# Optimization experiments

Hardware: AMD Instinct MI355X
Metric: run time of the kernel (lower is better)

Reference implementation:

```python
import jax, jax.numpy as jnp
import numpy as np

B, H, W, C = 8, 256, 256, 64
M1, M2 = 16, 16
WIDTH = 64
W_SCALE = 0.02  # mimics he-normal-ish init magnitude for complex spectral weights


def setup_inputs() -> dict:
    key = jax.random.key(0)
    k1, k2, k3 = jax.random.split(key, 3)
    x = jax.random.normal(k1, (B, H, W, C), dtype=jnp.float32)
    w_real = jax.random.normal(k2, (M1, M2, C, WIDTH), dtype=jnp.float32)
    w_imag = jax.random.normal(k3, (M1, M2, C, WIDTH), dtype=jnp.float32)
    return {"x": x, "w_real": w_real, "w_imag": w_imag}


def reference(x, w_real, w_imag):
    # complex spectral weights: (M1, M2, C_in, C_out)
    weights = (w_real + 1j * w_imag) * W_SCALE
    spatial = x.shape[1:-1]  # (H, W)
    # full real FFT over spatial axes -> (B, H, W//2+1, C) complex
    x_ft = jnp.fft.rfftn(x, axes=(1, 2))
    # truncate to low-frequency modes
    x_m = x_ft[:, :M1, :M2, :]  # (B, M1, M2, C)
    # per-mode channel mixing (broadcast-ellipsis einsum in the original)
    out_m = jnp.einsum("bxyi,xyio->bxyo", x_m, weights)  # (B, M1, M2, WIDTH)
    # zero-pad back to full spectral grid
    pad = ((0, 0), (0, x_ft.shape[1] - M1), (0, x_ft.shape[2] - M2), (0, 0))
    out_ft = jnp.pad(out_m, pad, mode="constant")
    # inverse real FFT back to spatial domain
    out = jnp.fft.irfftn(out_ft, s=spatial, axes=(1, 2))  # (B, H, W, WIDTH)
    return out
```

## Files before the change

### kernel.cpp

```cpp
#include <hip/hip_runtime.h>


#define NB 8
#define NH 256
#define NW 256
#define NC 64
#define NM 16
#define NO 64

__global__ __launch_bounds__(256) void k_dft_w(const float* __restrict__ x,
                                               float* __restrict__ Gr, float* __restrict__ Gi) {
  __shared__ float2 cs[256];
  const int t = threadIdx.x;
  {
    float s, c;
    sincospif((float)t * (1.0f / 128.0f), &s, &c);
    cs[t] = make_float2(c, s);
  }
  __syncthreads();
  const int b = blockIdx.x >> 7;
  const int h2 = blockIdx.x & 127;
  const int i4 = t & 15;
  const int hs = (t >> 4) & 1;
  const int kyq = t >> 5;
  const int ky0 = kyq * 2, ky1 = ky0 + 1;
  const int h = h2 * 2 + hs;
  const float* xp = x + ((size_t)(b * NH + h) * NW) * NC + i4 * 4;

  float4 ar0 = {0, 0, 0, 0}, ai0 = {0, 0, 0, 0}, ar1 = {0, 0, 0, 0}, ai1 = {0, 0, 0, 0};
  const float2 s0 = cs[ky0], s1 = cs[ky1];
  const float s0r = s0.x, s0i = -s0.y, s1r = s1.x, s1i = -s1.y;

  for (int wc = 0; wc < 8; ++wc) {
    const int w0 = wc * 32;
    const float2 v0 = cs[(ky0 * w0) & 255], v1 = cs[(ky1 * w0) & 255];
    float t0r = v0.x, t0i = -v0.y, t1r = v1.x, t1i = -v1.y;
#pragma unroll 8
    for (int w = 0; w < 32; ++w) {
      const float4 xv = *(const float4*)(xp + (size_t)(w0 + w) * NC);
      ar0.x += t0r * xv.x; ar0.y += t0r * xv.y; ar0.z += t0r * xv.z; ar0.w += t0r * xv.w;
      ai0.x += t0i * xv.x; ai0.y += t0i * xv.y; ai0.z += t0i * xv.z; ai0.w += t0i * xv.w;
      ar1.x += t1r * xv.x; ar1.y += t1r * xv.y; ar1.z += t1r * xv.z; ar1.w += t1r * xv.w;
      ai1.x += t1i * xv.x; ai1.y += t1i * xv.y; ai1.z += t1i * xv.z; ai1.w += t1i * xv.w;
      float n0r = t0r * s0r - t0i * s0i, n0i = t0r * s0i + t0i * s0r;
      float n1r = t1r * s1r - t1i * s1i, n1i = t1r * s1i + t1i * s1r;
      t0r = n0r; t0i = n0i; t1r = n1r; t1i = n1i;
    }
  }
  const size_t g0 = ((size_t)(b * NM + ky0) * NH + h) * NC + i4 * 4;
  const size_t g1 = ((size_t)(b * NM + ky1) * NH + h) * NC + i4 * 4;
  *(float4*)(Gr + g0) = ar0; *(float4*)(Gi + g0) = ai0;
  *(float4*)(Gr + g1) = ar1; *(float4*)(Gi + g1) = ai1;
}

__global__ __launch_bounds__(256) void k_dft_h(const float* __restrict__ Gr, const float* __restrict__ Gi,
                                               float* __restrict__ Xpr, float* __restrict__ Xpi) {
  __shared__ float2 cs[256];
  __shared__ float gr[32 * 64];
  __shared__ float gi[32 * 64];
  const int t = threadIdx.x;
  {
    float s, c;
    sincospif((float)t * (1.0f / 128.0f), &s, &c);
    cs[t] = make_float2(c, s);
  }
  const int b = blockIdx.x >> 7;
  const int ky = (blockIdx.x >> 3) & 15;
  const int hc = blockIdx.x & 7;
  const float* grs = Gr + ((size_t)(b * NM + ky) * NH + hc * 32) * NC;
  const float* gis = Gi + ((size_t)(b * NM + ky) * NH + hc * 32) * NC;
#pragma unroll
  for (int r = 0; r < 2; ++r) {
    ((float4*)gr)[r * 256 + t] = ((const float4*)grs)[r * 256 + t];
    ((float4*)gi)[r * 256 + t] = ((const float4*)gis)[r * 256 + t];
  }
  __syncthreads();
  const int i4 = t & 15;
  const int kx = t >> 4;
  float4 xr = {0, 0, 0, 0}, xi = {0, 0, 0, 0};
  const float2 sv = cs[kx];
  const float str = sv.x, sti = -sv.y;
  const float2 tv = cs[(kx * hc * 32) & 255];
  float twr = tv.x, twi = -tv.y;
#pragma unroll 4
  for (int hh = 0; hh < 32; ++hh) {
    const float4 g_r = *(const float4*)&gr[hh * 64 + i4 * 4];
    const float4 g_i = *(const float4*)&gi[hh * 64 + i4 * 4];
    xr.x += twr * g_r.x - twi * g_i.x;
    xr.y += twr * g_r.y - twi * g_i.y;
    xr.z += twr * g_r.z - twi * g_i.z;
    xr.w += twr * g_r.w - twi * g_i.w;
    xi.x += twr * g_i.x + twi * g_r.x;
    xi.y += twr * g_i.y + twi * g_r.y;
    xi.z += twr * g_i.z + twi * g_r.z;
    xi.w += twr * g_i.w + twi * g_r.w;
    const float nr = twr * str - twi * sti;
    const float ni = twr * sti + twi * str;
    twr = nr; twi = ni;
  }
  const size_t o = ((size_t)((hc * NM + kx) * NM + ky) * NB + b) * NC + i4 * 4;
  *(float4*)(Xpr + o) = xr;
  *(float4*)(Xpi + o) = xi;
}

__global__ __launch_bounds__(256) void k_mix(const float* __restrict__ Xpr, const float* __restrict__ Xpi,
                                             const float* __restrict__ w_real, const float* __restrict__ w_imag,
                                             float2* __restrict__ om) {
  __shared__ float wr_s[64 * 32];
  __shared__ float wi_s[64 * 32];
  __shared__ float2 xc[8 * 64];
  const int t = threadIdx.x;
  const int kx = blockIdx.x >> 5;
  const int ky = (blockIdx.x >> 1) & 15;
  const int oh = blockIdx.x & 1;
  const size_t wb = (size_t)(kx * NM + ky) * 4096 + oh * 32;
#pragma unroll
  for (int r = 0; r < 2; ++r) {
    const int idx = r * 256 + t;
    const int i = idx >> 3, f = idx & 7;
    *(float4*)&wr_s[i * 32 + f * 4] = *(const float4*)(w_real + wb + (size_t)i * 64 + f * 4);
    *(float4*)&wi_s[i * 32 + f * 4] = *(const float4*)(w_imag + wb + (size_t)i * 64 + f * 4);
  }
#pragma unroll
  for (int r = 0; r < 2; ++r) {
    const int idx = r * 256 + t;
    const size_t base = (size_t)(kx * NM + ky) * 512 + idx;
    float sr = 0.f, si = 0.f;
#pragma unroll
    for (int hc = 0; hc < 8; ++hc) {
      sr += Xpr[base + (size_t)hc * 131072];
      si += Xpi[base + (size_t)hc * 131072];
    }
    xc[idx] = make_float2(sr, si);
  }
  __syncthreads();
  const int o = t & 31;
  const int b = t >> 5;
  float r0 = 0.f, i0 = 0.f;
#pragma unroll 8
  for (int i = 0; i < 64; ++i) {
    const float2 xv = xc[b * 64 + i];
    const float wrv = wr_s[i * 32 + o];
    const float wiv = wi_s[i * 32 + o];
    r0 += xv.x * wrv - xv.y * wiv;
    i0 += xv.x * wiv + xv.y * wrv;
  }
  const float sc = (ky == 0 ? 1.0f : 2.0f) * (0.02f / 65536.0f);
  om[((size_t)(b * NM + kx) * NM + ky) * NO + oh * 32 + o] = make_float2(r0 * sc, i0 * sc);
}

__global__ __launch_bounds__(256) void k_idft_w(const float2* __restrict__ om, float2* __restrict__ Zc) {
  __shared__ float2 cs[256];
  const int t = threadIdx.x;
  {
    float s, c;
    sincospif((float)t * (1.0f / 128.0f), &s, &c);
    cs[t] = make_float2(c, s);
  }
  __syncthreads();
  const int b = blockIdx.x >> 7;
  const int kx = (blockIdx.x >> 3) & 15;
  const int wq = blockIdx.x & 7;
  const int o = t & 63;
  const int wg = t >> 6;
  float mr[16], mi[16];
  const size_t base = ((size_t)(b * NM + kx) * NM) * NO + o;
#pragma unroll
  for (int ky = 0; ky < NM; ++ky) {
    const float2 v = om[base + ky * NO];
    mr[ky] = v.x; mi[ky] = v.y;
  }
#pragma unroll
  for (int j = 0; j < 8; ++j) {
    const int w = wq * 32 + wg * 8 + j;
    const float2 st = cs[w];
    float twr = 1.0f, twi = 0.0f;
    float zr = 0.0f, zi = 0.0f;
#pragma unroll
    for (int ky = 0; ky < NM; ++ky) {
      zr += twr * mr[ky] - twi * mi[ky];
      zi += twr * mi[ky] + twi * mr[ky];
      const float nr = twr * st.x - twi * st.y;
      const float ni = twr * st.y + twi * st.x;
      twr = nr; twi = ni;
    }
    Zc[((size_t)(b * NW + w) * NM + kx) * NO + o] = make_float2(zr, zi);
  }
}

__global__ __launch_bounds__(256) void k_idft_h(const float2* __restrict__ Zc, float* __restrict__ out) {
  __shared__ float2 cs[256];
  __shared__ float zre[16 * 64];
  __shared__ float zim[16 * 64];
  const int t = threadIdx.x;
  {
    float s, c;
    sincospif((float)t * (1.0f / 128.0f), &s, &c);
    cs[t] = make_float2(c, s);
  }
  const int b = blockIdx.x >> 9;
  const int w = (blockIdx.x >> 1) & 255;
  const int hh = blockIdx.x & 1;
  const float4* src = (const float4*)(Zc + (size_t)(b * NW + w) * (NM * NO));
#pragma unroll
  for (int r = 0; r < 2; ++r) {
    const int idx = r * 256 + t;
    const float4 v = src[idx];
    ((float2*)zre)[idx] = make_float2(v.x, v.z);
    ((float2*)zim)[idx] = make_float2(v.y, v.w);
  }
  __syncthreads();
  const int i4 = t & 15;
  const int hg = t >> 4;
  const int h0 = hh * 128 + hg * 8;
  float4 acc[8];
#pragma unroll
  for (int j = 0; j < 8; ++j) acc[j] = make_float4(0, 0, 0, 0);
#pragma unroll 4
  for (int kx = 0; kx < 16; ++kx) {
    const float4 zr4 = ((const float4*)zre)[kx * 16 + i4];
    const float4 zi4 = ((const float4*)zim)[kx * 16 + i4];
    const float2 t0 = cs[(kx * h0) & 255];
    const float2 st = cs[kx];
    float twr = t0.x, twi = t0.y;
#pragma unroll
    for (int j = 0; j < 8; ++j) {
      acc[j].x += twr * zr4.x - twi * zi4.x;
      acc[j].y += twr * zr4.y - twi * zi4.y;
      acc[j].z += twr * zr4.z - twi * zi4.z;
      acc[j].w += twr * zr4.w - twi * zi4.w;
      const float nr = twr * st.x - twi * st.y;
      const float ni = twr * st.y + twi * st.x;
      twr = nr; twi = ni;
    }
  }
  float* ob = out + (((size_t)(b * NH) + h0) * NW + w) * NO + i4 * 4;
#pragma unroll
  for (int j = 0; j < 8; ++j) {
    *(float4*)(ob + (size_t)j * (NW * NO)) = acc[j];
  }
}

extern "C" void kernel_launch(void* const* d_in, const int* in_sizes, int n_in,
                              void* d_out, int out_size, void* d_ws, size_t ws_size,
                              hipStream_t stream) {
  const float* x = (const float*)d_in[0];
  const float* w_real = (const float*)d_in[1];
  const float* w_imag = (const float*)d_in[2];
  float* out = (float*)d_out;
  char* ws = (char*)d_ws;

  float* Gr = (float*)(ws);
  float* Gi = (float*)(ws + 8388608);
  float* Xpr = (float*)(ws + 16777216);
  float* Xpi = (float*)(ws + 20971520);
  float2* om = (float2*)(ws + 25165824);
  float2* Zc = (float2*)(ws);

  k_dft_w<<<dim3(1024), dim3(256), 0, stream>>>(x, Gr, Gi);
  k_dft_h<<<dim3(1024), dim3(256), 0, stream>>>(Gr, Gi, Xpr, Xpi);
  k_mix<<<dim3(512), dim3(256), 0, stream>>>(Xpr, Xpi, w_real, w_imag, om);
  k_idft_w<<<dim3(1024), dim3(256), 0, stream>>>(om, Zc);
  k_idft_h<<<dim3(4096), dim3(256), 0, stream>>>(Zc, out);
}
```

Measured before the change: 308.9 us.

## Fuse inverse DFT stages and stage forward W-DFT input through LDS

The forward W-direction DFT now gives each block one full input row. That row is streamed into double-buffered shared memory with global_load_lds, the W range is split between half-waves, and the partial sums are combined by shuffle. The two inverse DFT kernels are merged into one: each block computes the W-inverse for a single column into LDS and then does the H-inverse directly, so the Zc intermediate no longer round-trips through global memory. In exchange the mode coefficients are recomputed per block, and there are more syncs per chunk.

```diff
diff --git a/kernel.cpp b/kernel.cpp
--- a/kernel.cpp
+++ b/kernel.cpp
@@ -8,49 +8,83 @@
 #define NM 16
 #define NO 64
 
+__device__ __forceinline__ void gload16(const float* g, float* l) {
+  __builtin_amdgcn_global_load_lds(
+      (const __attribute__((address_space(1))) void*)g,
+      (__attribute__((address_space(3))) void*)l, 16, 0, 0);
+}
+
 __global__ __launch_bounds__(256) void k_dft_w(const float* __restrict__ x,
                                                float* __restrict__ Gr, float* __restrict__ Gi) {
   __shared__ float2 cs[256];
+  __shared__ float xs[2][2048];
   const int t = threadIdx.x;
   {
     float s, c;
     sincospif((float)t * (1.0f / 128.0f), &s, &c);
     cs[t] = make_float2(c, s);
   }
-  __syncthreads();
-  const int b = blockIdx.x >> 7;
-  const int h2 = blockIdx.x & 127;
+  const int b = blockIdx.x >> 8;
+  const int h = blockIdx.x & 255;
+  const float* row = x + (size_t)(b * NH + h) * (NW * NC);
+
+  const int wv = t >> 6;
+  {
+    const float* g0 = row + t * 4;
+    gload16(g0, &xs[0][wv * 256]);
+    gload16(g0 + 1024, &xs[0][1024 + wv * 256]);
+  }
+
   const int i4 = t & 15;
-  const int hs = (t >> 4) & 1;
-  const int kyq = t >> 5;
-  const int ky0 = kyq * 2, ky1 = ky0 + 1;
-  const int h = h2 * 2 + hs;
-  const float* xp = x + ((size_t)(b * NH + h) * NW) * NC + i4 * 4;
+  const int wh = (t >> 4) & 1;
+  const int kyp = t >> 5;
+  const int ky0 = kyp * 2, ky1 = ky0 + 1;
+
+  __syncthreads();
+
+  const float2 s0v = cs[ky0], s1v = cs[ky1];
+  const float s0r = s0v.x, s0i = -s0v.y, s1r = s1v.x, s1i = -s1v.y;
 
   float4 ar0 = {0, 0, 0, 0}, ai0 = {0, 0, 0, 0}, ar1 = {0, 0, 0, 0}, ai1 = {0, 0, 0, 0};
-  const float2 s0 = cs[ky0], s1 = cs[ky1];
-  const float s0r = s0.x, s0i = -s0.y, s1r = s1.x, s1i = -s1.y;
-
-  for (int wc = 0; wc < 8; ++wc) {
-    const int w0 = wc * 32;
-    const float2 v0 = cs[(ky0 * w0) & 255], v1 = cs[(ky1 * w0) & 255];
-    float t0r = v0.x, t0i = -v0.y, t1r = v1.x, t1i = -v1.y;
-#pragma unroll 8
-    for (int w = 0; w < 32; ++w) {
-      const float4 xv = *(const float4*)(xp + (size_t)(w0 + w) * NC);
+  int buf = 0;
+  for (int c = 0; c < 8; ++c) {
+    if (c < 7) {
+      const float* g0 = row + (c + 1) * 2048 + t * 4;
+      gload16(g0, &xs[buf ^ 1][wv * 256]);
+      gload16(g0 + 1024, &xs[buf ^ 1][1024 + wv * 256]);
+    }
+    const int w0 = c * 32 + wh * 16;
+    const float2 u0 = cs[(ky0 * w0) & 255];
+    const float2 u1 = cs[(ky1 * w0) & 255];
+    float t0r = u0.x, t0i = -u0.y, t1r = u1.x, t1i = -u1.y;
+    const float* xb = &xs[buf][wh * 1024 + i4 * 4];
+#pragma unroll
+    for (int ww = 0; ww < 16; ++ww) {
+      const float4 xv = *(const float4*)(xb + ww * 64);
       ar0.x += t0r * xv.x; ar0.y += t0r * xv.y; ar0.z += t0r * xv.z; ar0.w += t0r * xv.w;
       ai0.x += t0i * xv.x; ai0.y += t0i * xv.y; ai0.z += t0i * xv.z; ai0.w += t0i * xv.w;
       ar1.x += t1r * xv.x; ar1.y += t1r * xv.y; ar1.z += t1r * xv.z; ar1.w += t1r * xv.w;
       ai1.x += t1i * xv.x; ai1.y += t1i * xv.y; ai1.z += t1i * xv.z; ai1.w += t1i * xv.w;
-      float n0r = t0r * s0r - t0i * s0i, n0i = t0r * s0i + t0i * s0r;
-      float n1r = t1r * s1r - t1i * s1i, n1i = t1r * s1i + t1i * s1r;
+      const float n0r = t0r * s0r - t0i * s0i, n0i = t0r * s0i + t0i * s0r;
+      const float n1r = t1r * s1r - t1i * s1i, n1i = t1r * s1i + t1i * s1r;
       t0r = n0r; t0i = n0i; t1r = n1r; t1i = n1i;
     }
-  }
-  const size_t g0 = ((size_t)(b * NM + ky0) * NH + h) * NC + i4 * 4;
-  const size_t g1 = ((size_t)(b * NM + ky1) * NH + h) * NC + i4 * 4;
-  *(float4*)(Gr + g0) = ar0; *(float4*)(Gi + g0) = ai0;
-  *(float4*)(Gr + g1) = ar1; *(float4*)(Gi + g1) = ai1;
+    __syncthreads();
+    buf ^= 1;
+  }
+
+#define RED4(v)                                                         \
+  v.x += __shfl_xor(v.x, 16); v.y += __shfl_xor(v.y, 16);               \
+  v.z += __shfl_xor(v.z, 16); v.w += __shfl_xor(v.w, 16);
+  RED4(ar0) RED4(ai0) RED4(ar1) RED4(ai1)
+#undef RED4
+
+  if (wh == 0) {
+    const size_t g0 = ((size_t)(b * NM + ky0) * NH + h) * NC + i4 * 4;
+    const size_t g1 = ((size_t)(b * NM + ky1) * NH + h) * NC + i4 * 4;
+    *(float4*)(Gr + g0) = ar0; *(float4*)(Gi + g0) = ai0;
+    *(float4*)(Gr + g1) = ar1; *(float4*)(Gi + g1) = ai1;
+  }
 }
 
 __global__ __launch_bounds__(256) void k_dft_h(const float* __restrict__ Gr, const float* __restrict__ Gi,
@@ -149,95 +183,78 @@
   om[((size_t)(b * NM + kx) * NM + ky) * NO + oh * 32 + o] = make_float2(r0 * sc, i0 * sc);
 }
 
-__global__ __launch_bounds__(256) void k_idft_w(const float2* __restrict__ om, float2* __restrict__ Zc) {
+#define ZLD 72
+__global__ __launch_bounds__(256) void k_idft_we(const float2* __restrict__ om, float* __restrict__ out) {
   __shared__ float2 cs[256];
+  __shared__ float zre[NM * ZLD];
+  __shared__ float zim[NM * ZLD];
   const int t = threadIdx.x;
   {
     float s, c;
     sincospif((float)t * (1.0f / 128.0f), &s, &c);
     cs[t] = make_float2(c, s);
   }
-  __syncthreads();
-  const int b = blockIdx.x >> 7;
-  const int kx = (blockIdx.x >> 3) & 15;
-  const int wq = blockIdx.x & 7;
-  const int o = t & 63;
-  const int wg = t >> 6;
-  float mr[16], mi[16];
-  const size_t base = ((size_t)(b * NM + kx) * NM) * NO + o;
-#pragma unroll
-  for (int ky = 0; ky < NM; ++ky) {
-    const float2 v = om[base + ky * NO];
-    mr[ky] = v.x; mi[ky] = v.y;
-  }
-#pragma unroll
-  for (int j = 0; j < 8; ++j) {
-    const int w = wq * 32 + wg * 8 + j;
+  const int b = blockIdx.x >> 8;
+  const int w = blockIdx.x & 255;
+  __syncthreads();
+
+  {
+    const int kx = t >> 4;
+    const int og = t & 15;
+    const float2* mp = om + ((size_t)(b * NM + kx) * NM) * NO + og * 4;
+    float zr[4] = {0, 0, 0, 0}, zi[4] = {0, 0, 0, 0};
     const float2 st = cs[w];
     float twr = 1.0f, twi = 0.0f;
-    float zr = 0.0f, zi = 0.0f;
 #pragma unroll
     for (int ky = 0; ky < NM; ++ky) {
-      zr += twr * mr[ky] - twi * mi[ky];
-      zi += twr * mi[ky] + twi * mr[ky];
+      const float2 m0 = mp[(size_t)ky * NO + 0];
+      const float2 m1 = mp[(size_t)ky * NO + 1];
+      const float2 m2 = mp[(size_t)ky * NO + 2];
+      const float2 m3 = mp[(size_t)ky * NO + 3];
+      zr[0] += twr * m0.x - twi * m0.y; zi[0] += twr * m0.y + twi * m0.x;
+      zr[1] += twr * m1.x - twi * m1.y; zi[1] += twr * m1.y + twi * m1.x;
+      zr[2] += twr * m2.x - twi * m2.y; zi[2] += twr * m2.y + twi * m2.x;
+      zr[3] += twr * m3.x - twi * m3.y; zi[3] += twr * m3.y + twi * m3.x;
       const float nr = twr * st.x - twi * st.y;
       const float ni = twr * st.y + twi * st.x;
       twr = nr; twi = ni;
     }
-    Zc[((size_t)(b * NW + w) * NM + kx) * NO + o] = make_float2(zr, zi);
-  }
-}
-
-__global__ __launch_bounds__(256) void k_idft_h(const float2* __restrict__ Zc, float* __restrict__ out) {
-  __shared__ float2 cs[256];
-  __shared__ float zre[16 * 64];
-  __shared__ float zim[16 * 64];
-  const int t = threadIdx.x;
-  {
-    float s, c;
-    sincospif((float)t * (1.0f / 128.0f), &s, &c);
-    cs[t] = make_float2(c, s);
-  }
-  const int b = blockIdx.x >> 9;
-  const int w = (blockIdx.x >> 1) & 255;
-  const int hh = blockIdx.x & 1;
-  const float4* src = (const float4*)(Zc + (size_t)(b * NW + w) * (NM * NO));
-#pragma unroll
-  for (int r = 0; r < 2; ++r) {
-    const int idx = r * 256 + t;
-    const float4 v = src[idx];
-    ((float2*)zre)[idx] = make_float2(v.x, v.z);
-    ((float2*)zim)[idx] = make_float2(v.y, v.w);
-  }
-  __syncthreads();
+    *(float4*)&zre[kx * ZLD + og * 4] = make_float4(zr[0], zr[1], zr[2], zr[3]);
+    *(float4*)&zim[kx * ZLD + og * 4] = make_float4(zi[0], zi[1], zi[2], zi[3]);
+  }
+  __syncthreads();
+
   const int i4 = t & 15;
   const int hg = t >> 4;
-  const int h0 = hh * 128 + hg * 8;
-  float4 acc[8];
-#pragma unroll
-  for (int j = 0; j < 8; ++j) acc[j] = make_float4(0, 0, 0, 0);
+#pragma unroll
+  for (int hh = 0; hh < 2; ++hh) {
+    const int h0 = hh * 128 + hg * 8;
+    float4 acc[8];
+#pragma unroll
+    for (int j = 0; j < 8; ++j) acc[j] = make_float4(0, 0, 0, 0);
 #pragma unroll 4
-  for (int kx = 0; kx < 16; ++kx) {
-    const float4 zr4 = ((const float4*)zre)[kx * 16 + i4];
-    const float4 zi4 = ((const float4*)zim)[kx * 16 + i4];
-    const float2 t0 = cs[(kx * h0) & 255];
-    const float2 st = cs[kx];
-    float twr = t0.x, twi = t0.y;
+    for (int kx = 0; kx < 16; ++kx) {
+      const float4 zr4 = *(const float4*)&zre[kx * ZLD + i4 * 4];
+      const float4 zi4 = *(const float4*)&zim[kx * ZLD + i4 * 4];
+      const float2 t0 = cs[(kx * h0) & 255];
+      const float2 st = cs[kx];
+      float twr = t0.x, twi = t0.y;
+#pragma unroll
+      for (int j = 0; j < 8; ++j) {
+        acc[j].x += twr * zr4.x - twi * zi4.x;
+        acc[j].y += twr * zr4.y - twi * zi4.y;
+        acc[j].z += twr * zr4.z - twi * zi4.z;
+        acc[j].w += twr * zr4.w - twi * zi4.w;
+        const float nr = twr * st.x - twi * st.y;
+        const float ni = twr * st.y + twi * st.x;
+        twr = nr; twi = ni;
+      }
+    }
+    float* ob = out + (((size_t)(b * NH) + h0) * NW + w) * NO + i4 * 4;
 #pragma unroll
     for (int j = 0; j < 8; ++j) {
-      acc[j].x += twr * zr4.x - twi * zi4.x;
-      acc[j].y += twr * zr4.y - twi * zi4.y;
-      acc[j].z += twr * zr4.z - twi * zi4.z;
-      acc[j].w += twr * zr4.w - twi * zi4.w;
-      const float nr = twr * st.x - twi * st.y;
-      const float ni = twr * st.y + twi * st.x;
-      twr = nr; twi = ni;
-    }
-  }
-  float* ob = out + (((size_t)(b * NH) + h0) * NW + w) * NO + i4 * 4;
-#pragma unroll
-  for (int j = 0; j < 8; ++j) {
-    *(float4*)(ob + (size_t)j * (NW * NO)) = acc[j];
+      *(float4*)(ob + (size_t)j * (NW * NO)) = acc[j];
+    }
   }
 }
 
@@ -255,11 +272,9 @@
   float* Xpr = (float*)(ws + 16777216);
   float* Xpi = (float*)(ws + 20971520);
   float2* om = (float2*)(ws + 25165824);
-  float2* Zc = (float2*)(ws);
-
-  k_dft_w<<<dim3(1024), dim3(256), 0, stream>>>(x, Gr, Gi);
+
+  k_dft_w<<<dim3(2048), dim3(256), 0, stream>>>(x, Gr, Gi);
   k_dft_h<<<dim3(1024), dim3(256), 0, stream>>>(Gr, Gi, Xpr, Xpi);
   k_mix<<<dim3(512), dim3(256), 0, stream>>>(Xpr, Xpi, w_real, w_imag, om);
-  k_idft_w<<<dim3(1024), dim3(256), 0, stream>>>(om, Zc);
-  k_idft_h<<<dim3(4096), dim3(256), 0, stream>>>(Zc, out);
-}
+  k_idft_we<<<dim3(2048), dim3(256), 0, stream>>>(om, out);
+}
```

Result: no change. 307.3 us (-0.5%).
